# Performance work log

Hardware: AMD Instinct MI355X
Metric: run time of the kernel (lower is better)

Reference implementation:

```python
import jax, jax.numpy as jnp
import numpy as np

SEQ_LEN = 2048
D_MODEL = 1024
D_KEY = 64
BATCH = 8


def setup_inputs() -> dict:
    key = jax.random.key(0)
    ks = jax.random.split(key, 7)
    s = 1.0 / np.sqrt(D_MODEL)
    return {
        "input": jax.random.normal(ks[0], (BATCH, SEQ_LEN, D_MODEL), dtype=jnp.float32),
        "Wq": jax.random.uniform(ks[1], (D_MODEL, D_KEY), jnp.float32, -s, s),
        "bq": jax.random.uniform(ks[2], (D_KEY,), jnp.float32, -s, s),
        "Wk": jax.random.uniform(ks[3], (D_MODEL, D_KEY), jnp.float32, -s, s),
        "bk": jax.random.uniform(ks[4], (D_KEY,), jnp.float32, -s, s),
        "Wv": jax.random.uniform(ks[5], (D_MODEL, D_MODEL), jnp.float32, -s, s),
        "bv": jax.random.uniform(ks[6], (D_MODEL,), jnp.float32, -s, s),
    }


def reference(input, Wq, bq, Wk, bk, Wv, bv):
    # single-head causal attention with full score materialization
    q = input @ Wq + bq                      # [B, S, dk]
    k = input @ Wk + bk                      # [B, S, dk]
    v = input @ Wv + bv                      # [B, S, dm]
    scale = jnp.sqrt(jnp.asarray(D_KEY, input.dtype))
    scores = jnp.einsum("bqd,bkd->bqk", q, k) / scale   # [B, S, S]
    causal = jnp.tril(jnp.ones((SEQ_LEN, SEQ_LEN), dtype=bool))
    scores = jnp.where(causal[None, :, :], scores, -jnp.inf)
    attn = jax.nn.softmax(scores, axis=-1)
    return jnp.einsum("bqk,bkd->bqd", attn, v)           # [B, S, dm]
```

## Files before the change

### kernel.cpp

```cpp
#include <hip/hip_runtime.h>
#include <math.h>

#define B 8
#define S 2048
#define DM 1024
#define DK 64
#define M_ROWS (B*S)

typedef short s8v __attribute__((ext_vector_type(8)));
typedef float f4v __attribute__((ext_vector_type(4)));
typedef unsigned short us4 __attribute__((ext_vector_type(4)));

__device__ __forceinline__ unsigned short f2bf(float f) {
    union { float f; unsigned u; } v; v.f = f;
    unsigned r = v.u + 0x7fffu + ((v.u >> 16) & 1u);
    return (unsigned short)(r >> 16);
}
__device__ __forceinline__ s8v ld8(const unsigned short* p) {
    return *(const s8v*)p;
}
__device__ __forceinline__ f4v mf16(s8v a, s8v b, f4v c) {
    return __builtin_amdgcn_mfma_f32_16x16x32_bf16(a, b, c, 0, 0, 0);
}
__device__ __forceinline__ void gload16(const unsigned short* g, unsigned short* l) {
    __builtin_amdgcn_global_load_lds(
        (const __attribute__((address_space(1))) void*)g,
        (__attribute__((address_space(3))) void*)l, 16, 0, 0);
}
__device__ __forceinline__ void bar_lgkm() {
    asm volatile("s_waitcnt lgkmcnt(0)" ::: "memory");
    __builtin_amdgcn_s_barrier();
}

__global__ __launch_bounds__(256) void cast_x(const float* __restrict__ x,
                                              unsigned short* __restrict__ xb) {
    size_t i = ((size_t)blockIdx.x * 256 + threadIdx.x) * 4;
    float4 v = *(const float4*)(x + i);
    us4 o; o.x = f2bf(v.x); o.y = f2bf(v.y); o.z = f2bf(v.z); o.w = f2bf(v.w);
    *(us4*)(xb + i) = o;
}

__global__ __launch_bounds__(256) void wv_t(const float* __restrict__ Wv,
                                            unsigned short* __restrict__ Wvt) {
    __shared__ float T[32][33];
    int t = threadIdx.x;
    int k0 = blockIdx.y * 32, n0 = blockIdx.x * 32;
    int r = t >> 3, c = (t & 7) * 4;
    float4 v = *(const float4*)(Wv + (size_t)(k0 + r) * DM + n0 + c);
    T[r][c + 0] = v.x; T[r][c + 1] = v.y; T[r][c + 2] = v.z; T[r][c + 3] = v.w;
    __syncthreads();
    us4 o;
    o.x = f2bf(T[c + 0][r]); o.y = f2bf(T[c + 1][r]);
    o.z = f2bf(T[c + 2][r]); o.w = f2bf(T[c + 3][r]);
    *(us4*)(Wvt + (size_t)(n0 + r) * DM + k0 + c) = o;
}

__global__ __launch_bounds__(256) void wqk_t(const float* __restrict__ Wq,
                                             const float* __restrict__ Wk,
                                             unsigned short* __restrict__ Wqkt) {
    __shared__ float T[32][33];
    int t = threadIdx.x;
    int k0 = blockIdx.y * 32, n0 = blockIdx.x * 32;
    const float* src = (n0 < 64) ? Wq : Wk;
    int nc = (n0 < 64) ? n0 : (n0 - 64);
    int r = t >> 3, c = (t & 7) * 4;
    float4 v = *(const float4*)(src + (size_t)(k0 + r) * DK + nc + c);
    T[r][c + 0] = v.x; T[r][c + 1] = v.y; T[r][c + 2] = v.z; T[r][c + 3] = v.w;
    __syncthreads();
    us4 o;
    o.x = f2bf(T[c + 0][r]); o.y = f2bf(T[c + 1][r]);
    o.z = f2bf(T[c + 2][r]); o.w = f2bf(T[c + 3][r]);
    *(us4*)(Wqkt + (size_t)(n0 + r) * DM + k0 + c) = o;
}

__global__ __launch_bounds__(256) void qk_mfma(
        const unsigned short* __restrict__ xb,
        const unsigned short* __restrict__ Wqkt,
        const float* __restrict__ bq, const float* __restrict__ bk,
        unsigned short* __restrict__ Q, unsigned short* __restrict__ Ko) {
    __shared__ unsigned short XS[64 * 64];
    __shared__ unsigned short WS[128 * 64];
    int t = threadIdx.x;
    int w = t >> 6, lane = t & 63, l16 = lane & 15, quad = lane >> 4;
    int m0 = blockIdx.x * 64;
    int wm = (w >> 1) * 32, wn = (w & 1) * 64;
    f4v acc[2][4] = {};
    int srow = w * 8 + (lane >> 3);
    int scol = ((lane & 7) ^ (srow & 7)) * 8;
    int soff = w * 512 + lane * 8;
    for (int k0 = 0; k0 < DM; k0 += 64) {
        __syncthreads();
        #pragma unroll
        for (int i = 0; i < 2; ++i)
            gload16(xb + (size_t)(m0 + i * 32 + srow) * DM + k0 + scol,
                    XS + i * 2048 + soff);
        #pragma unroll
        for (int i = 0; i < 4; ++i)
            gload16(Wqkt + (size_t)(i * 32 + srow) * DM + k0 + scol,
                    WS + i * 2048 + soff);
        __syncthreads();
        #pragma unroll
        for (int ks = 0; ks < 2; ++ks) {
            s8v af[2], bf[4];
            #pragma unroll
            for (int i = 0; i < 2; ++i) {
                int r = wm + i * 16 + l16;
                af[i] = *(const s8v*)&XS[r * 64 + ((ks * 4 + quad) ^ (r & 7)) * 8];
            }
            #pragma unroll
            for (int j = 0; j < 4; ++j) {
                int r = wn + j * 16 + l16;
                bf[j] = *(const s8v*)&WS[r * 64 + ((ks * 4 + quad) ^ (r & 7)) * 8];
            }
            #pragma unroll
            for (int i = 0; i < 2; ++i)
                #pragma unroll
                for (int j = 0; j < 4; ++j)
                    acc[i][j] = mf16(af[i], bf[j], acc[i][j]);
        }
    }
    #pragma unroll
    for (int j = 0; j < 4; ++j) {
        int n = wn + j * 16 + l16;
        float bias = (n < 64) ? bq[n] : bk[n - 64];
        float scale = (n < 64) ? 0.125f : 1.0f;
        unsigned short* dst = (n < 64) ? Q : Ko;
        int nn = n & 63;
        #pragma unroll
        for (int i = 0; i < 2; ++i)
            #pragma unroll
            for (int rr = 0; rr < 4; ++rr) {
                int m = m0 + wm + i * 16 + quad * 4 + rr;
                dst[(size_t)m * DK + nn] = f2bf((acc[i][j][rr] + bias) * scale);
            }
    }
}

__global__ __launch_bounds__(256) void v_proj_mfma(
        const unsigned short* __restrict__ xb,
        const unsigned short* __restrict__ Wvt,
        const float* __restrict__ bv,
        unsigned short* __restrict__ Vt) {
    __shared__ unsigned short XS[128 * 64];
    __shared__ unsigned short WS[128 * 64];
    int t = threadIdx.x;
    int w = t >> 6, lane = t & 63, l16 = lane & 15, quad = lane >> 4;
    int m0 = blockIdx.y * 128, n0 = blockIdx.x * 128;
    int wm = (w >> 1) * 64, wn = (w & 1) * 64;
    f4v acc[4][4] = {};
    int srow = w * 8 + (lane >> 3);
    int scol = ((lane & 7) ^ (srow & 7)) * 8;
    int soff = w * 512 + lane * 8;
    for (int k0 = 0; k0 < DM; k0 += 64) {
        __syncthreads();
        #pragma unroll
        for (int i = 0; i < 4; ++i) {
            gload16(xb  + (size_t)(m0 + i * 32 + srow) * DM + k0 + scol,
                    XS + i * 2048 + soff);
            gload16(Wvt + (size_t)(n0 + i * 32 + srow) * DM + k0 + scol,
                    WS + i * 2048 + soff);
        }
        __syncthreads();
        #pragma unroll
        for (int ks = 0; ks < 2; ++ks) {
            s8v af[4], bf[4];
            #pragma unroll
            for (int i = 0; i < 4; ++i) {
                int r = wm + i * 16 + l16;
                af[i] = *(const s8v*)&XS[r * 64 + ((ks * 4 + quad) ^ (r & 7)) * 8];
            }
            #pragma unroll
            for (int j = 0; j < 4; ++j) {
                int r = wn + j * 16 + l16;
                bf[j] = *(const s8v*)&WS[r * 64 + ((ks * 4 + quad) ^ (r & 7)) * 8];
            }
            #pragma unroll
            for (int i = 0; i < 4; ++i)
                #pragma unroll
                for (int j = 0; j < 4; ++j)
                    acc[i][j] = mf16(af[i], bf[j], acc[i][j]);
        }
    }
    int bb = m0 >> 11;
    #pragma unroll
    for (int j = 0; j < 4; ++j) {
        int n = n0 + wn + j * 16 + l16;
        float bias = bv[n];
        #pragma unroll
        for (int i = 0; i < 4; ++i) {
            int m = m0 + wm + i * 16 + quad * 4;
            int s = m & (S - 1);
            us4 o;
            o.x = f2bf(acc[i][j][0] + bias); o.y = f2bf(acc[i][j][1] + bias);
            o.z = f2bf(acc[i][j][2] + bias); o.w = f2bf(acc[i][j][3] + bias);
            *(us4*)(Vt + ((size_t)bb * DM + n) * S + s) = o;
        }
    }
}

__global__ __launch_bounds__(256, 2) void attn_mfma(
        const unsigned short* __restrict__ Q,
        const unsigned short* __restrict__ K,
        const unsigned short* __restrict__ Vt,
        float* __restrict__ out) {
    __shared__ unsigned short KS[64][64];
    __shared__ unsigned short VS[2][128][64];
    __shared__ unsigned short PS[128][64];
    __shared__ float lS[128];

    int t = threadIdx.x;
    int w = t >> 6, lane = t & 63;
    int l16 = lane & 15, hi = lane >> 4;
    int b = blockIdx.z;
    int dm0 = blockIdx.x * 128;
    int wn = w * 32;

    int krow = t >> 3, kc = t & 7;
    int voff = w * 512 + lane * 8;
    int vrow = w * 8 + (lane >> 3);
    int vcol = ((lane & 7) ^ (vrow & 7)) * 8;

    const unsigned short* Kb = K  + (size_t)b * S * DK;
    const unsigned short* Vb = Vt + ((size_t)b * DM + dm0) * S;

    #pragma unroll 1
    for (int half = 0; half < 2; ++half) {
        int qidx = half ? (15 - (int)blockIdx.y) : (int)blockIdx.y;
        int q0 = qidx * 128;
        int NJ = q0 + 128;
        int qw = q0 + w * 32;

        s8v qf[2][2];
        #pragma unroll
        for (int qh = 0; qh < 2; ++qh)
            #pragma unroll
            for (int ks = 0; ks < 2; ++ks)
                qf[qh][ks] = ld8(Q + ((size_t)b * S + qw + qh * 16 + l16) * DK
                                   + ks * 32 + hi * 8);

        float lacc[2] = {0.f, 0.f};
        f4v acc[8][2] = {};

        {
            s8v kr0 = ld8(Kb + (size_t)krow * DK + kc * 8);
            s8v kr1 = ld8(Kb + (size_t)(krow + 32) * DK + kc * 8);
            #pragma unroll
            for (int rep = 0; rep < 4; ++rep)
                gload16(Vb + (size_t)(rep * 32 + vrow) * S + vcol,
                        &VS[0][0][0] + rep * 2048 + voff);
            *(s8v*)&KS[krow][(kc ^ (krow & 7)) * 8] = kr0;
            *(s8v*)&KS[krow + 32][(kc ^ (krow & 7)) * 8] = kr1;
        }
        __syncthreads();

        int cur = 0;
        for (int j0 = 0; j0 < NJ; j0 += 64) {
            int jn = j0 + 64;
            bool pf = jn < NJ;
            s8v kp0, kp1;
            if (pf) {
                kp0 = ld8(Kb + (size_t)(jn + krow) * DK + kc * 8);
                kp1 = ld8(Kb + (size_t)(jn + krow + 32) * DK + kc * 8);
                #pragma unroll
                for (int rep = 0; rep < 4; ++rep)
                    gload16(Vb + (size_t)(rep * 32 + vrow) * S + jn + vcol,
                            &VS[cur ^ 1][0][0] + rep * 2048 + voff);
            }
            #pragma unroll
            for (int jt = 0; jt < 4; ++jt) {
                int jrow = jt * 16 + l16;
                s8v ka0 = *(const s8v*)&KS[jrow][((0 + hi) ^ (jrow & 7)) * 8];
                s8v ka1 = *(const s8v*)&KS[jrow][((4 + hi) ^ (jrow & 7)) * 8];
                #pragma unroll
                for (int qh = 0; qh < 2; ++qh) {
                    f4v d = {0.f, 0.f, 0.f, 0.f};
                    d = mf16(ka0, qf[qh][0], d);
                    d = mf16(ka1, qf[qh][1], d);
                    int qg = qw + qh * 16 + l16;
                    int jbase = j0 + jt * 16 + hi * 4;
                    float p0 = (jbase + 0 <= qg) ? __expf(d[0]) : 0.f;
                    float p1 = (jbase + 1 <= qg) ? __expf(d[1]) : 0.f;
                    float p2 = (jbase + 2 <= qg) ? __expf(d[2]) : 0.f;
                    float p3 = (jbase + 3 <= qg) ? __expf(d[3]) : 0.f;
                    lacc[qh] += (p0 + p1) + (p2 + p3);
                    us4 pk;
                    pk.x = f2bf(p0); pk.y = f2bf(p1); pk.z = f2bf(p2); pk.w = f2bf(p3);
                    int prow = w * 32 + qh * 16 + l16;
                    int pc = jt * 2 + (hi >> 1);
                    *(us4*)&PS[prow][((pc ^ (prow & 7)) * 8) + (hi & 1) * 4] = pk;
                }
            }
            bar_lgkm();
            if (pf) {
                *(s8v*)&KS[krow][(kc ^ (krow & 7)) * 8] = kp0;
                *(s8v*)&KS[krow + 32][(kc ^ (krow & 7)) * 8] = kp1;
            }
            __builtin_amdgcn_s_setprio(1);
            #pragma unroll
            for (int js = 0; js < 2; ++js) {
                s8v pa[8];
                #pragma unroll
                for (int qt = 0; qt < 8; ++qt) {
                    int qr = qt * 16 + l16;
                    pa[qt] = *(const s8v*)&PS[qr][((js * 4 + hi) ^ (qr & 7)) * 8];
                }
                #pragma unroll
                for (int nt = 0; nt < 2; ++nt) {
                    int nr = wn + nt * 16 + l16;
                    s8v vb = *(const s8v*)&VS[cur][nr][((js * 4 + hi) ^ (nr & 7)) * 8];
                    #pragma unroll
                    for (int qt = 0; qt < 8; ++qt)
                        acc[qt][nt] = mf16(pa[qt], vb, acc[qt][nt]);
                }
            }
            __builtin_amdgcn_s_setprio(0);
            __syncthreads();
            cur ^= 1;
        }

        #pragma unroll
        for (int qh = 0; qh < 2; ++qh) {
            float lt = lacc[qh];
            lt += __shfl_xor(lt, 16);
            lt += __shfl_xor(lt, 32);
            if (hi == 0) lS[w * 32 + qh * 16 + l16] = lt;
        }
        __syncthreads();

        #pragma unroll
        for (int qt = 0; qt < 8; ++qt) {
            f4v lv = *(const f4v*)&lS[qt * 16 + hi * 4];
            f4v inv;
            inv[0] = 1.f / lv[0]; inv[1] = 1.f / lv[1];
            inv[2] = 1.f / lv[2]; inv[3] = 1.f / lv[3];
            size_t rbase = (size_t)b * S + q0 + qt * 16 + hi * 4;
            #pragma unroll
            for (int nt = 0; nt < 2; ++nt)
                #pragma unroll
                for (int r = 0; r < 4; ++r)
                    out[(rbase + r) * DM + dm0 + wn + nt * 16 + l16] =
                        acc[qt][nt][r] * inv[r];
        }
        __syncthreads();
    }
}

extern "C" void kernel_launch(void* const* d_in, const int* in_sizes, int n_in,
                              void* d_out, int out_size, void* d_ws, size_t ws_size,
                              hipStream_t stream) {
    const float* x  = (const float*)d_in[0];
    const float* Wq = (const float*)d_in[1];
    const float* bq = (const float*)d_in[2];
    const float* Wk = (const float*)d_in[3];
    const float* bk = (const float*)d_in[4];
    const float* Wv = (const float*)d_in[5];
    const float* bv = (const float*)d_in[6];
    float* out = (float*)d_out;

    unsigned short* xb   = (unsigned short*)d_ws;
    unsigned short* Wvt  = xb   + (size_t)M_ROWS * DM;
    unsigned short* Qb   = Wvt  + (size_t)DM * DM;
    unsigned short* Kb   = Qb   + (size_t)M_ROWS * DK;
    unsigned short* Vt   = Kb   + (size_t)M_ROWS * DK;
    unsigned short* Wqkt = Vt   + (size_t)B * DM * S;

    cast_x<<<(size_t)M_ROWS * DM / 1024, 256, 0, stream>>>(x, xb);
    wv_t<<<dim3(32, 32), 256, 0, stream>>>(Wv, Wvt);
    wqk_t<<<dim3(4, 32), 256, 0, stream>>>(Wq, Wk, Wqkt);
    qk_mfma<<<M_ROWS / 64, 256, 0, stream>>>(xb, Wqkt, bq, bk, Qb, Kb);
    v_proj_mfma<<<dim3(DM / 128, M_ROWS / 128), 256, 0, stream>>>(xb, Wvt, bv, Vt);
    attn_mfma<<<dim3(DM / 128, 8, B), 256, 0, stream>>>(Qb, Kb, Vt, out);
}
```

Baseline: 291.1 us.

## Widen attention tile to 256 dm columns with 512 threads and register K

```diff
diff --git a/kernel.cpp b/kernel.cpp
--- a/kernel.cpp
+++ b/kernel.cpp
@@ -26,10 +26,6 @@
     __builtin_amdgcn_global_load_lds(
         (const __attribute__((address_space(1))) void*)g,
         (__attribute__((address_space(3))) void*)l, 16, 0, 0);
-}
-__device__ __forceinline__ void bar_lgkm() {
-    asm volatile("s_waitcnt lgkmcnt(0)" ::: "memory");
-    __builtin_amdgcn_s_barrier();
 }
 
 __global__ __launch_bounds__(256) void cast_x(const float* __restrict__ x,
@@ -198,118 +194,115 @@
     }
 }
 
-__global__ __launch_bounds__(256, 2) void attn_mfma(
+__global__ __launch_bounds__(512, 2) void attn_mfma(
         const unsigned short* __restrict__ Q,
         const unsigned short* __restrict__ K,
         const unsigned short* __restrict__ Vt,
         float* __restrict__ out) {
-    __shared__ unsigned short KS[64][64];
-    __shared__ unsigned short VS[2][128][64];
     __shared__ unsigned short PS[128][64];
     __shared__ float lS[128];
+    __shared__ unsigned short VS[2][256][64];
 
     int t = threadIdx.x;
     int w = t >> 6, lane = t & 63;
     int l16 = lane & 15, hi = lane >> 4;
-    int b = blockIdx.z;
-    int dm0 = blockIdx.x * 128;
-    int wn = w * 32;
-
-    int krow = t >> 3, kc = t & 7;
-    int voff = w * 512 + lane * 8;
-    int vrow = w * 8 + (lane >> 3);
-    int vcol = ((lane & 7) ^ (vrow & 7)) * 8;
+    int bid = blockIdx.x;
+    int b  = bid & 7;
+    int bx = (bid >> 3) & 3;
+    int by = bid >> 5;
+    int dm0 = bx * 256;
+    int wn = (w & 3) * 64;
+    int qg = (w >> 2) * 64;
+
+    int vrow = t >> 3;
+    int voff = t * 8;
+    int gcol = ((t & 7) ^ ((t >> 3) & 7)) * 8;
 
     const unsigned short* Kb = K  + (size_t)b * S * DK;
     const unsigned short* Vb = Vt + ((size_t)b * DM + dm0) * S;
+    const unsigned short* kbase = Kb + (size_t)l16 * DK + hi * 8;
 
     #pragma unroll 1
     for (int half = 0; half < 2; ++half) {
-        int qidx = half ? (15 - (int)blockIdx.y) : (int)blockIdx.y;
+        int qidx = half ? (15 - by) : by;
         int q0 = qidx * 128;
         int NJ = q0 + 128;
-        int qw = q0 + w * 32;
-
-        s8v qf[2][2];
-        #pragma unroll
-        for (int qh = 0; qh < 2; ++qh)
+        int qw = q0 + w * 16;
+
+        s8v qf[2];
+        #pragma unroll
+        for (int ks = 0; ks < 2; ++ks)
+            qf[ks] = ld8(Q + ((size_t)b * S + qw + l16) * DK + ks * 32 + hi * 8);
+
+        float lacc = 0.f;
+        f4v acc[4][4] = {};
+
+        s8v ka[8];
+        #pragma unroll
+        for (int rep = 0; rep < 4; ++rep)
+            gload16(Vb + (size_t)(rep * 64 + vrow) * S + gcol,
+                    &VS[0][0][0] + rep * 4096 + voff);
+        #pragma unroll
+        for (int jt = 0; jt < 4; ++jt)
             #pragma unroll
             for (int ks = 0; ks < 2; ++ks)
-                qf[qh][ks] = ld8(Q + ((size_t)b * S + qw + qh * 16 + l16) * DK
-                                   + ks * 32 + hi * 8);
-
-        float lacc[2] = {0.f, 0.f};
-        f4v acc[8][2] = {};
-
-        {
-            s8v kr0 = ld8(Kb + (size_t)krow * DK + kc * 8);
-            s8v kr1 = ld8(Kb + (size_t)(krow + 32) * DK + kc * 8);
-            #pragma unroll
-            for (int rep = 0; rep < 4; ++rep)
-                gload16(Vb + (size_t)(rep * 32 + vrow) * S + vcol,
-                        &VS[0][0][0] + rep * 2048 + voff);
-            *(s8v*)&KS[krow][(kc ^ (krow & 7)) * 8] = kr0;
-            *(s8v*)&KS[krow + 32][(kc ^ (krow & 7)) * 8] = kr1;
-        }
+                ka[jt * 2 + ks] = ld8(kbase + (size_t)(jt * 16) * DK + ks * 32);
         __syncthreads();
 
         int cur = 0;
         for (int j0 = 0; j0 < NJ; j0 += 64) {
             int jn = j0 + 64;
             bool pf = jn < NJ;
-            s8v kp0, kp1;
             if (pf) {
-                kp0 = ld8(Kb + (size_t)(jn + krow) * DK + kc * 8);
-                kp1 = ld8(Kb + (size_t)(jn + krow + 32) * DK + kc * 8);
                 #pragma unroll
                 for (int rep = 0; rep < 4; ++rep)
-                    gload16(Vb + (size_t)(rep * 32 + vrow) * S + jn + vcol,
-                            &VS[cur ^ 1][0][0] + rep * 2048 + voff);
+                    gload16(Vb + (size_t)(rep * 64 + vrow) * S + jn + gcol,
+                            &VS[cur ^ 1][0][0] + rep * 4096 + voff);
             }
             #pragma unroll
             for (int jt = 0; jt < 4; ++jt) {
-                int jrow = jt * 16 + l16;
-                s8v ka0 = *(const s8v*)&KS[jrow][((0 + hi) ^ (jrow & 7)) * 8];
-                s8v ka1 = *(const s8v*)&KS[jrow][((4 + hi) ^ (jrow & 7)) * 8];
-                #pragma unroll
-                for (int qh = 0; qh < 2; ++qh) {
-                    f4v d = {0.f, 0.f, 0.f, 0.f};
-                    d = mf16(ka0, qf[qh][0], d);
-                    d = mf16(ka1, qf[qh][1], d);
-                    int qg = qw + qh * 16 + l16;
-                    int jbase = j0 + jt * 16 + hi * 4;
-                    float p0 = (jbase + 0 <= qg) ? __expf(d[0]) : 0.f;
-                    float p1 = (jbase + 1 <= qg) ? __expf(d[1]) : 0.f;
-                    float p2 = (jbase + 2 <= qg) ? __expf(d[2]) : 0.f;
-                    float p3 = (jbase + 3 <= qg) ? __expf(d[3]) : 0.f;
-                    lacc[qh] += (p0 + p1) + (p2 + p3);
-                    us4 pk;
-                    pk.x = f2bf(p0); pk.y = f2bf(p1); pk.z = f2bf(p2); pk.w = f2bf(p3);
-                    int prow = w * 32 + qh * 16 + l16;
-                    int pc = jt * 2 + (hi >> 1);
-                    *(us4*)&PS[prow][((pc ^ (prow & 7)) * 8) + (hi & 1) * 4] = pk;
-                }
-            }
-            bar_lgkm();
+                f4v d = {0.f, 0.f, 0.f, 0.f};
+                d = mf16(ka[jt * 2 + 0], qf[0], d);
+                d = mf16(ka[jt * 2 + 1], qf[1], d);
+                int qglob = qw + l16;
+                int jbase = j0 + jt * 16 + hi * 4;
+                float p0 = (jbase + 0 <= qglob) ? __expf(d[0]) : 0.f;
+                float p1 = (jbase + 1 <= qglob) ? __expf(d[1]) : 0.f;
+                float p2 = (jbase + 2 <= qglob) ? __expf(d[2]) : 0.f;
+                float p3 = (jbase + 3 <= qglob) ? __expf(d[3]) : 0.f;
+                lacc += (p0 + p1) + (p2 + p3);
+                unsigned r0, r1;
+                asm("v_cvt_pk_bf16_f32 %0, %1, %2" : "=v"(r0) : "v"(p0), "v"(p1));
+                asm("v_cvt_pk_bf16_f32 %0, %1, %2" : "=v"(r1) : "v"(p2), "v"(p3));
+                int prow = w * 16 + l16;
+                int pc = jt * 2 + (hi >> 1);
+                uint2 pk2; pk2.x = r0; pk2.y = r1;
+                *(uint2*)&PS[prow][((pc ^ (prow & 7)) * 8) + (hi & 1) * 4] = pk2;
+            }
             if (pf) {
-                *(s8v*)&KS[krow][(kc ^ (krow & 7)) * 8] = kp0;
-                *(s8v*)&KS[krow + 32][(kc ^ (krow & 7)) * 8] = kp1;
-            }
+                #pragma unroll
+                for (int jt = 0; jt < 4; ++jt)
+                    #pragma unroll
+                    for (int ks = 0; ks < 2; ++ks)
+                        ka[jt * 2 + ks] =
+                            ld8(kbase + (size_t)(jn + jt * 16) * DK + ks * 32);
+            }
+            __syncthreads();
             __builtin_amdgcn_s_setprio(1);
             #pragma unroll
             for (int js = 0; js < 2; ++js) {
-                s8v pa[8];
-                #pragma unroll
-                for (int qt = 0; qt < 8; ++qt) {
-                    int qr = qt * 16 + l16;
+                s8v pa[4];
+                #pragma unroll
+                for (int qt = 0; qt < 4; ++qt) {
+                    int qr = qg + qt * 16 + l16;
                     pa[qt] = *(const s8v*)&PS[qr][((js * 4 + hi) ^ (qr & 7)) * 8];
                 }
                 #pragma unroll
-                for (int nt = 0; nt < 2; ++nt) {
+                for (int nt = 0; nt < 4; ++nt) {
                     int nr = wn + nt * 16 + l16;
                     s8v vb = *(const s8v*)&VS[cur][nr][((js * 4 + hi) ^ (nr & 7)) * 8];
                     #pragma unroll
-                    for (int qt = 0; qt < 8; ++qt)
+                    for (int qt = 0; qt < 4; ++qt)
                         acc[qt][nt] = mf16(pa[qt], vb, acc[qt][nt]);
                 }
             }
@@ -318,24 +311,23 @@
             cur ^= 1;
         }
 
-        #pragma unroll
-        for (int qh = 0; qh < 2; ++qh) {
-            float lt = lacc[qh];
+        {
+            float lt = lacc;
             lt += __shfl_xor(lt, 16);
             lt += __shfl_xor(lt, 32);
-            if (hi == 0) lS[w * 32 + qh * 16 + l16] = lt;
-        }
-        __syncthreads();
-
-        #pragma unroll
-        for (int qt = 0; qt < 8; ++qt) {
-            f4v lv = *(const f4v*)&lS[qt * 16 + hi * 4];
+            if (hi == 0) lS[w * 16 + l16] = lt;
+        }
+        __syncthreads();
+
+        #pragma unroll
+        for (int qt = 0; qt < 4; ++qt) {
+            f4v lv = *(const f4v*)&lS[qg + qt * 16 + hi * 4];
             f4v inv;
             inv[0] = 1.f / lv[0]; inv[1] = 1.f / lv[1];
             inv[2] = 1.f / lv[2]; inv[3] = 1.f / lv[3];
-            size_t rbase = (size_t)b * S + q0 + qt * 16 + hi * 4;
-            #pragma unroll
-            for (int nt = 0; nt < 2; ++nt)
+            size_t rbase = (size_t)b * S + q0 + qg + qt * 16 + hi * 4;
+            #pragma unroll
+            for (int nt = 0; nt < 4; ++nt)
                 #pragma unroll
                 for (int r = 0; r < 4; ++r)
                     out[(rbase + r) * DM + dm0 + wn + nt * 16 + l16] =
@@ -369,5 +361,5 @@
     wqk_t<<<dim3(4, 32), 256, 0, stream>>>(Wq, Wk, Wqkt);
     qk_mfma<<<M_ROWS / 64, 256, 0, stream>>>(xb, Wqkt, bq, bk, Qb, Kb);
     v_proj_mfma<<<dim3(DM / 128, M_ROWS / 128), 256, 0, stream>>>(xb, Wvt, bv, Vt);
-    attn_mfma<<<dim3(DM / 128, 8, B), 256, 0, stream>>>(Qb, Kb, Vt, out);
-}
+    attn_mfma<<<dim3(256), 512, 0, stream>>>(Qb, Kb, Vt, out);
+}
```

Measured after the change: 280.4 us. 1.04x faster.
